# Kernel optimization log

Measured on AMD Instinct MI355X. Metric: run time of the kernel, lower is better.

The kernel has to match this reference:

```python
import jax, jax.numpy as jnp
import numpy as np

B, T, C, H = 4, 2048, 1024, 16
NEG = -1e9  # masked-fill value (finite to keep grads clean)


def setup_inputs() -> dict:
    key = jax.random.key(0)
    ks = jax.random.split(key, 5)
    s = 1.0 / np.sqrt(C)  # keep logits O(1) like trained linear layers
    return {
        "x": jax.random.normal(ks[0], (B, T, C), dtype=jnp.float32),
        "wq": jax.random.normal(ks[1], (C, C), dtype=jnp.float32) * s,
        "bq": jnp.zeros((C,), dtype=jnp.float32),
        "wk": jax.random.normal(ks[2], (C, C), dtype=jnp.float32) * s,
        "bk": jnp.zeros((C,), dtype=jnp.float32),
        "wv": jax.random.normal(ks[3], (C, C), dtype=jnp.float32) * s,
        "bv": jnp.zeros((C,), dtype=jnp.float32),
        "wo": jax.random.normal(ks[4], (C, C), dtype=jnp.float32) * s,
        "bo": jnp.zeros((C,), dtype=jnp.float32),
    }


def _split_heads(y):
    # [B,T,C] -> [B,H,T,hd]
    b, t, c = y.shape
    return y.reshape(b, t, H, c // H).transpose(0, 2, 1, 3)


def reference(x, wq, bq, wk, bk, wv, bv, wo, bo):
    b, t, c = x.shape
    scale = (c // H) ** (-0.5)
    q = _split_heads(x @ wq.T + bq)  # [B,H,T,hd]
    k = _split_heads(x @ wk.T + bk)
    v = _split_heads(x @ wv.T + bv)
    att = jnp.einsum("bhqd,bhkd->bhqk", q, k) * scale  # [B,H,T,T]
    causal = jnp.tril(jnp.ones((t, t), dtype=bool))
    att = jnp.where(causal[None, None], att, NEG)
    att = jax.nn.softmax(att, axis=-1)  # dropout is identity in eval mode
    y = jnp.einsum("bhqk,bhkd->bhqd", att, v)
    y = y.transpose(0, 2, 1, 3).reshape(b, t, c)
    return y @ wo.T + bo
```

## Files before the change

### kernel.cpp

```cpp
#include <hip/hip_runtime.h>


#define B_ 4
#define T_ 2048
#define C_ 1024
#define H_ 16
#define M_ 8192

typedef unsigned short u16;
typedef __bf16 bf16x8 __attribute__((ext_vector_type(8)));
typedef float f32x4 __attribute__((ext_vector_type(4)));

static __device__ __forceinline__ u16 f2bf(float f) {
  unsigned int u = __float_as_uint(f);
  u += 0x7fffu + ((u >> 16) & 1u);
  return (u16)(u >> 16);
}

static __device__ __forceinline__ void async16(const void* g, void* l) {
  __builtin_amdgcn_global_load_lds(
      (const __attribute__((address_space(1))) unsigned int*)g,
      (__attribute__((address_space(3))) unsigned int*)l, 16, 0, 0);
}

#if __has_builtin(__builtin_amdgcn_exp2f)
#define EXP2F(x) __builtin_amdgcn_exp2f(x)
#else
#define EXP2F(x) exp2f(x)
#endif

static __device__ __forceinline__ f32x4 mfma32(bf16x8 a, bf16x8 b, f32x4 c) {
  return __builtin_amdgcn_mfma_f32_16x16x32_bf16(a, b, c, 0, 0, 0);
}

__global__ __launch_bounds__(256) void cvt_x(const float* __restrict__ src,
                                             u16* __restrict__ dst, int n4) {
  int i = blockIdx.x * 256 + threadIdx.x;
  if (i >= n4) return;
  float4 f = ((const float4*)src)[i];
  ushort4 o;
  o.x = f2bf(f.x); o.y = f2bf(f.y); o.z = f2bf(f.z); o.w = f2bf(f.w);
  ((ushort4*)dst)[i] = o;
}

__global__ __launch_bounds__(256) void cvt_w4(const float* __restrict__ w0,
                                              const float* __restrict__ w1,
                                              const float* __restrict__ w2,
                                              const float* __restrict__ w3,
                                              u16* __restrict__ o0, u16* __restrict__ o1,
                                              u16* __restrict__ o2, u16* __restrict__ o3,
                                              float s0) {
  int i = blockIdx.x * 256 + threadIdx.x;
  const float* src; u16* dst; float s = 1.f;
  switch (blockIdx.y) {
    case 0: src = w0; dst = o0; s = s0; break;
    case 1: src = w1; dst = o1; break;
    case 2: src = w2; dst = o2; break;
    default: src = w3; dst = o3; break;
  }
  float4 f = ((const float4*)src)[i];
  ushort4 o;
  o.x = f2bf(f.x * s); o.y = f2bf(f.y * s); o.z = f2bf(f.z * s); o.w = f2bf(f.w * s);
  ((ushort4*)dst)[i] = o;
}

__global__ __launch_bounds__(256, 4) void gemm_qkv(const u16* __restrict__ A,
                                                   const u16* __restrict__ W,
                                                   const float* __restrict__ bq,
                                                   const float* __restrict__ bk,
                                                   const float* __restrict__ bv,
                                                   float qscale,
                                                   u16* __restrict__ outqk,
                                                   u16* __restrict__ vtb) {
  __shared__ __align__(16) union {
    struct { u16 A[128 * 64]; u16 B[128 * 64]; } s;
    u16 C[128 * 136];
  } sm;
  const int tid = threadIdx.x, lane = tid & 63, wave = tid >> 6;
  const int quad = lane >> 4, l16 = lane & 15;
  const int wm = wave >> 1, wn = wave & 1;
  const int sel = blockIdx.x >> 3;
  const int col0 = (blockIdx.x & 7) * 128, row0 = blockIdx.y * 128;
  const u16* Bt = W + (size_t)sel * C_ * C_;
  const float* bias = sel == 0 ? bq : (sel == 1 ? bk : bv);
  const float bscale = sel == 0 ? qscale : 1.f;

  f32x4 zero = {0.f, 0.f, 0.f, 0.f};
  f32x4 acc[4][4];
#pragma unroll
  for (int i = 0; i < 4; i++)
#pragma unroll
    for (int j = 0; j < 4; j++) acc[i][j] = zero;

  for (int k0 = 0; k0 < C_; k0 += 64) {
#pragma unroll
    for (int i = 0; i < 4; i++) {
      int c = i * 256 + tid;
      int r = c >> 3, gcc = (c & 7) ^ (r & 7);
      async16(A + (size_t)(row0 + r) * C_ + k0 + gcc * 8,
              sm.s.A + (size_t)(i * 256 + wave * 64) * 8);
      async16(Bt + (size_t)(col0 + r) * C_ + k0 + gcc * 8,
              sm.s.B + (size_t)(i * 256 + wave * 64) * 8);
    }
    __syncthreads();

#pragma unroll
    for (int kk = 0; kk < 2; kk++) {
      bf16x8 a[4], b[4];
#pragma unroll
      for (int i = 0; i < 4; i++) {
        int rm = wm * 64 + 16 * i + l16;
        a[i] = *(const bf16x8*)(sm.s.A + rm * 64 + (((kk * 4 + quad) ^ (rm & 7)) * 8));
        int rn = wn * 64 + 16 * i + l16;
        b[i] = *(const bf16x8*)(sm.s.B + rn * 64 + (((kk * 4 + quad) ^ (rn & 7)) * 8));
      }
#pragma unroll
      for (int i = 0; i < 4; i++)
#pragma unroll
        for (int j = 0; j < 4; j++)
          acc[i][j] = mfma32(a[i], b[j], acc[i][j]);
    }
    __syncthreads();
  }

  float bj[4];
#pragma unroll
  for (int j = 0; j < 4; j++) bj[j] = bias[col0 + wn * 64 + 16 * j + l16] * bscale;

  if (sel == 2) {
#pragma unroll
    for (int i = 0; i < 4; i++)
#pragma unroll
      for (int j = 0; j < 4; j++) {
        int cl = wn * 64 + 16 * j + l16;
        int rt = wm * 64 + 16 * i + quad * 4;
        union { u16 s[4]; uint2 u; } w;
#pragma unroll
        for (int r = 0; r < 4; r++) w.s[r] = f2bf(acc[i][j][r] + bj[j]);
        *(uint2*)(sm.C + (size_t)cl * 136 + rt) = w.u;
      }
    __syncthreads();
    const int bb = row0 >> 11, t0 = row0 & 2047;
#pragma unroll
    for (int c2 = 0; c2 < 8; c2++) {
      int c = c2 * 256 + tid;
      int nr = c >> 4, ch = c & 15;
      bf16x8 v = *(const bf16x8*)(sm.C + (size_t)nr * 136 + ch * 8);
      int gn = col0 + nr, d = gn & 63, hh = gn >> 6;
      *(bf16x8*)(vtb + ((size_t)((bb * 16 + hh) * 64 + d)) * T_ + t0 + ch * 8) = v;
    }
  } else {
#pragma unroll
    for (int i = 0; i < 4; i++)
#pragma unroll
      for (int j = 0; j < 4; j++) {
        int cl = wn * 64 + 16 * j + l16;
        int rt = wm * 64 + 16 * i + quad * 4;
#pragma unroll
        for (int r = 0; r < 4; r++)
          sm.C[(size_t)(rt + r) * 136 + cl] = f2bf(acc[i][j][r] + bj[j]);
      }
    __syncthreads();
    u16* dst = outqk + (size_t)sel * M_ * C_;
#pragma unroll
    for (int c2 = 0; c2 < 8; c2++) {
      int c = c2 * 256 + tid;
      int rw = c >> 4, ch = c & 15;
      bf16x8 v = *(const bf16x8*)(sm.C + (size_t)rw * 136 + ch * 8);
      *(bf16x8*)(dst + (size_t)(row0 + rw) * C_ + col0 + ch * 8) = v;
    }
  }
}

__global__ __launch_bounds__(256) void gemm_o(const u16* __restrict__ A,
                                              const u16* __restrict__ Bt,
                                              const float* __restrict__ bias,
                                              float* __restrict__ outf) {
  __shared__ __align__(16) u16 Asm[128 * 64];
  __shared__ __align__(16) u16 Bsm[128 * 64];
  const int tid = threadIdx.x, lane = tid & 63, wave = tid >> 6;
  const int quad = lane >> 4, l16 = lane & 15;
  const int wm = wave >> 1, wn = wave & 1;
  const int col0 = blockIdx.x * 128, row0 = blockIdx.y * 128;

  f32x4 zero = {0.f, 0.f, 0.f, 0.f};
  f32x4 acc[4][4];
#pragma unroll
  for (int i = 0; i < 4; i++)
#pragma unroll
    for (int j = 0; j < 4; j++) acc[i][j] = zero;

  for (int k0 = 0; k0 < C_; k0 += 64) {
#pragma unroll
    for (int i = 0; i < 4; i++) {
      int c = i * 256 + tid;
      int r = c >> 3, gcc = (c & 7) ^ (r & 7);
      async16(A + (size_t)(row0 + r) * C_ + k0 + gcc * 8,
              Asm + (size_t)(i * 256 + wave * 64) * 8);
      async16(Bt + (size_t)(col0 + r) * C_ + k0 + gcc * 8,
              Bsm + (size_t)(i * 256 + wave * 64) * 8);
    }
    __syncthreads();

#pragma unroll
    for (int kk = 0; kk < 2; kk++) {
      bf16x8 a[4], b[4];
#pragma unroll
      for (int i = 0; i < 4; i++) {
        int rm = wm * 64 + 16 * i + l16;
        a[i] = *(const bf16x8*)(Asm + rm * 64 + (((kk * 4 + quad) ^ (rm & 7)) * 8));
        int rn = wn * 64 + 16 * i + l16;
        b[i] = *(const bf16x8*)(Bsm + rn * 64 + (((kk * 4 + quad) ^ (rn & 7)) * 8));
      }
#pragma unroll
      for (int i = 0; i < 4; i++)
#pragma unroll
        for (int j = 0; j < 4; j++)
          acc[i][j] = mfma32(a[i], b[j], acc[i][j]);
    }
    __syncthreads();
  }

  float bj[4];
#pragma unroll
  for (int j = 0; j < 4; j++) bj[j] = bias[col0 + wn * 64 + 16 * j + l16];
#pragma unroll
  for (int i = 0; i < 4; i++) {
#pragma unroll
    for (int j = 0; j < 4; j++) {
      int gcol = col0 + wn * 64 + 16 * j + l16;
      int grow0 = row0 + wm * 64 + 16 * i + quad * 4;
#pragma unroll
      for (int r = 0; r < 4; r++)
        outf[(size_t)(grow0 + r) * C_ + gcol] = acc[i][j][r] + bj[j];
    }
  }
}

__global__ __launch_bounds__(256) void attn(const u16* __restrict__ q,
                                            const u16* __restrict__ k,
                                            const u16* __restrict__ vt,
                                            u16* __restrict__ y) {
  __shared__ __align__(16) u16 Ksm[64 * 64];
  __shared__ __align__(16) u16 Vsm[64 * 64];
  __shared__ __align__(16) u16 Psm[4][32 * 64];
  const int tid = threadIdx.x, lane = tid & 63, wave = tid >> 6;
  const int quad = lane >> 4, l16 = lane & 15;
  static const int qperm[16] = {15, 14, 11, 10, 12, 13, 8, 9, 3, 2, 7, 6, 0, 1, 4, 5};
  const int bh = blockIdx.x;
  const int qt = qperm[blockIdx.y];
  const int b = bh >> 4, h = bh & 15;
  const int jtN = 2 * qt + 2;
  const int jt_d = 2 * qt + (wave >> 1);

  bf16x8 qf[2][2];
#pragma unroll
  for (int m = 0; m < 2; m++) {
    const u16* qp =
        q + (size_t)(b * T_ + qt * 128 + wave * 32 + m * 16 + l16) * C_ + h * 64;
#pragma unroll
    for (int ks = 0; ks < 2; ks++)
      qf[m][ks] = *(const bf16x8*)(qp + ks * 32 + quad * 8);
  }

  f32x4 zero = {0.f, 0.f, 0.f, 0.f};
  f32x4 o[2][4];
  float lp[2][4];
#pragma unroll
  for (int m = 0; m < 2; m++) {
#pragma unroll
    for (int dt = 0; dt < 4; dt++) o[m][dt] = zero;
#pragma unroll
    for (int r = 0; r < 4; r++) lp[m][r] = 0.f;
  }

  const u16* kp[2];
  const u16* vp[2];
#pragma unroll
  for (int i = 0; i < 2; i++) {
    int c = i * 256 + tid;
    int r = c >> 3, lc = (c & 7) ^ (r & 7);
    kp[i] = k + (size_t)(b * T_ + r) * C_ + h * 64 + lc * 8;
    vp[i] = vt + (size_t)(bh * 64 + r) * T_ + lc * 8;
  }

  int qrel[2];
#pragma unroll
  for (int m = 0; m < 2; m++)
    qrel[m] = wave * 32 + m * 16 + quad * 4 - (wave >> 1) * 64 - l16;
  const int nlim0 = 2 * (wave & 1) + 1;

  u16* Pw = &Psm[wave][0];

#pragma unroll 1
  for (int jt = 0; jt < jtN; ++jt) {
#pragma unroll
    for (int i = 0; i < 2; i++) {
      async16(kp[i], Ksm + (size_t)(i * 256 + wave * 64) * 8);
      async16(vp[i], Vsm + (size_t)(i * 256 + wave * 64) * 8);
      kp[i] += (size_t)64 * C_;
      vp[i] += 64;
    }
    __syncthreads();

    if (jt <= jt_d) {
      const bool diag = (jt == jt_d);
#pragma unroll
      for (int n = 0; n < 4; ++n) {
        int rk = n * 16 + l16;
        bf16x8 kf0 = *(const bf16x8*)(Ksm + rk * 64 + ((quad ^ (rk & 7)) * 8));
        bf16x8 kf1 = *(const bf16x8*)(Ksm + rk * 64 + (((4 + quad) ^ (rk & 7)) * 8));
#pragma unroll
        for (int m = 0; m < 2; ++m) {
          if (!diag || n < nlim0 + m) {
            f32x4 s = mfma32(qf[m][0], kf0, zero);
            s = mfma32(qf[m][1], kf1, s);
            float e[4];
#pragma unroll
            for (int r = 0; r < 4; r++) e[r] = EXP2F(s[r]);
            if (diag) {
              int rmin = n * 16 - qrel[m];
#pragma unroll
              for (int r = 0; r < 4; r++)
                if (r < rmin) e[r] = 0.f;
            }
#pragma unroll
            for (int r = 0; r < 4; r++) {
              lp[m][r] += e[r];
              int qr = m * 16 + quad * 4 + r;
              Pw[qr * 64 + (((n * 2 + (l16 >> 3)) ^ (qr & 7)) * 8) + (l16 & 7)] =
                  f2bf(e[r]);
            }
          } else {
#pragma unroll
            for (int r = 0; r < 4; r++) {
              int qr = m * 16 + quad * 4 + r;
              Pw[qr * 64 + (((n * 2 + (l16 >> 3)) ^ (qr & 7)) * 8) + (l16 & 7)] = 0;
            }
          }
        }
      }
      bf16x8 pf[2][2];
#pragma unroll
      for (int m = 0; m < 2; m++)
#pragma unroll
        for (int ks = 0; ks < 2; ks++)
          pf[m][ks] = *(const bf16x8*)(Pw + (m * 16 + l16) * 64 +
                                       (((ks * 4 + quad) ^ (l16 & 7)) * 8));
#pragma unroll
      for (int dt = 0; dt < 4; ++dt) {
        int rv = dt * 16 + l16;
        bf16x8 vf0 = *(const bf16x8*)(Vsm + rv * 64 + ((quad ^ (rv & 7)) * 8));
        bf16x8 vf1 = *(const bf16x8*)(Vsm + rv * 64 + (((4 + quad) ^ (rv & 7)) * 8));
#pragma unroll
        for (int m = 0; m < 2; m++) {
          o[m][dt] = mfma32(pf[m][0], vf0, o[m][dt]);
          o[m][dt] = mfma32(pf[m][1], vf1, o[m][dt]);
        }
      }
    }
    __syncthreads();
  }

#pragma unroll
  for (int m = 0; m < 2; m++)
#pragma unroll
    for (int r = 0; r < 4; r++) {
      float v = lp[m][r];
      v += __shfl_xor(v, 1);
      v += __shfl_xor(v, 2);
      v += __shfl_xor(v, 4);
      v += __shfl_xor(v, 8);
      lp[m][r] = 1.f / v;
    }

#pragma unroll
  for (int m = 0; m < 2; m++)
#pragma unroll
    for (int r = 0; r < 4; r++) {
      int grow = b * T_ + qt * 128 + wave * 32 + m * 16 + quad * 4 + r;
#pragma unroll
      for (int dt = 0; dt < 4; dt++)
        y[(size_t)grow * C_ + h * 64 + dt * 16 + l16] = f2bf(o[m][dt][r] * lp[m][r]);
    }
}

extern "C" void kernel_launch(void* const* d_in, const int* in_sizes, int n_in,
                              void* d_out, int out_size, void* d_ws, size_t ws_size,
                              hipStream_t stream) {
  const float* x  = (const float*)d_in[0];
  const float* wq = (const float*)d_in[1];
  const float* bq = (const float*)d_in[2];
  const float* wk = (const float*)d_in[3];
  const float* bk = (const float*)d_in[4];
  const float* wv = (const float*)d_in[5];
  const float* bv = (const float*)d_in[6];
  const float* wo = (const float*)d_in[7];
  const float* bo = (const float*)d_in[8];
  float* out = (float*)d_out;

  const float QSCALE = 0.125f * 1.4426950408889634f;

  u16* xb  = (u16*)d_ws;
  u16* wqb = xb  + (size_t)M_ * C_;
  u16* wkb = wqb + (size_t)C_ * C_;
  u16* wvb = wkb + (size_t)C_ * C_;
  u16* wob = wvb + (size_t)C_ * C_;
  u16* qb  = wob + (size_t)C_ * C_;
  u16* kb  = qb  + (size_t)M_ * C_;
  u16* vtb = kb  + (size_t)M_ * C_;
  u16* yb  = xb;

  cvt_x<<<M_ * C_ / 4 / 256, 256, 0, stream>>>(x, xb, M_ * C_ / 4);
  cvt_w4<<<dim3(C_ * C_ / 4 / 256, 4), 256, 0, stream>>>(
      wq, wk, wv, wo, wqb, wkb, wvb, wob, QSCALE);

  gemm_qkv<<<dim3(24, M_ / 128), 256, 0, stream>>>(xb, wqb, bq, bk, bv, QSCALE,
                                                   qb, vtb);

  attn<<<dim3(B_ * H_, 16), 256, 0, stream>>>(qb, kb, vtb, yb);

  gemm_o<<<dim3(C_ / 128, M_ / 128), 256, 0, stream>>>(yb, wob, bo, out);
}
```

Baseline: 269.9 us.

## Widen attention KV tile to 128 keys and fuse conversion kernels into one

The attention kernel now loads 128 keys per iteration, split into two 64-key halves, instead of 64. This halves the number of loop iterations and the barrier pairs per query tile, and the causal diagonal logic is rebuilt around per-wave half-tile limits. Separately, the x and weight bf16 conversions are merged into a single launch to save one kernel launch. The larger shared K/V buffers raise LDS use per block, which may lower occupancy.

```diff
diff --git a/kernel.cpp b/kernel.cpp
--- a/kernel.cpp
+++ b/kernel.cpp
@@ -33,35 +33,34 @@
   return __builtin_amdgcn_mfma_f32_16x16x32_bf16(a, b, c, 0, 0, 0);
 }
 
-__global__ __launch_bounds__(256) void cvt_x(const float* __restrict__ src,
-                                             u16* __restrict__ dst, int n4) {
+__global__ __launch_bounds__(256) void cvt_all(const float* __restrict__ x,
+                                               const float* __restrict__ w0,
+                                               const float* __restrict__ w1,
+                                               const float* __restrict__ w2,
+                                               const float* __restrict__ w3,
+                                               u16* __restrict__ xb,
+                                               u16* __restrict__ wb,
+                                               float s0) {
+  const int NX = M_ * C_ / 4, NW = C_ * C_ / 4;
   int i = blockIdx.x * 256 + threadIdx.x;
-  if (i >= n4) return;
-  float4 f = ((const float4*)src)[i];
-  ushort4 o;
-  o.x = f2bf(f.x); o.y = f2bf(f.y); o.z = f2bf(f.z); o.w = f2bf(f.w);
-  ((ushort4*)dst)[i] = o;
-}
-
-__global__ __launch_bounds__(256) void cvt_w4(const float* __restrict__ w0,
-                                              const float* __restrict__ w1,
-                                              const float* __restrict__ w2,
-                                              const float* __restrict__ w3,
-                                              u16* __restrict__ o0, u16* __restrict__ o1,
-                                              u16* __restrict__ o2, u16* __restrict__ o3,
-                                              float s0) {
-  int i = blockIdx.x * 256 + threadIdx.x;
-  const float* src; u16* dst; float s = 1.f;
-  switch (blockIdx.y) {
-    case 0: src = w0; dst = o0; s = s0; break;
-    case 1: src = w1; dst = o1; break;
-    case 2: src = w2; dst = o2; break;
-    default: src = w3; dst = o3; break;
-  }
-  float4 f = ((const float4*)src)[i];
+  const float* src;
+  u16* dst;
+  int idx;
+  float s = 1.f;
+  if (i < NX) {
+    src = x; dst = xb; idx = i;
+  } else {
+    int j = i - NX;
+    int w = j / NW;
+    idx = j - w * NW;
+    src = (w == 0) ? w0 : (w == 1) ? w1 : (w == 2) ? w2 : w3;
+    dst = wb + (size_t)w * C_ * C_;
+    if (w == 0) s = s0;
+  }
+  float4 f = ((const float4*)src)[idx];
   ushort4 o;
   o.x = f2bf(f.x * s); o.y = f2bf(f.y * s); o.z = f2bf(f.z * s); o.w = f2bf(f.w * s);
-  ((ushort4*)dst)[i] = o;
+  ((ushort4*)dst)[idx] = o;
 }
 
 __global__ __launch_bounds__(256, 4) void gemm_qkv(const u16* __restrict__ A,
@@ -241,8 +240,8 @@
                                             const u16* __restrict__ k,
                                             const u16* __restrict__ vt,
                                             u16* __restrict__ y) {
-  __shared__ __align__(16) u16 Ksm[64 * 64];
-  __shared__ __align__(16) u16 Vsm[64 * 64];
+  __shared__ __align__(16) u16 Ksm[128 * 64];
+  __shared__ __align__(16) u16 Vsm[2][64 * 64];
   __shared__ __align__(16) u16 Psm[4][32 * 64];
   const int tid = threadIdx.x, lane = tid & 63, wave = tid >> 6;
   const int quad = lane >> 4, l16 = lane & 15;
@@ -250,8 +249,6 @@
   const int bh = blockIdx.x;
   const int qt = qperm[blockIdx.y];
   const int b = bh >> 4, h = bh & 15;
-  const int jtN = 2 * qt + 2;
-  const int jt_d = 2 * qt + (wave >> 1);
 
   bf16x8 qf[2][2];
 #pragma unroll
@@ -274,52 +271,66 @@
     for (int r = 0; r < 4; r++) lp[m][r] = 0.f;
   }
 
-  const u16* kp[2];
-  const u16* vp[2];
-#pragma unroll
-  for (int i = 0; i < 2; i++) {
+  const u16* kp[4];
+  const u16* vp[4];
+#pragma unroll
+  for (int i = 0; i < 4; i++) {
     int c = i * 256 + tid;
     int r = c >> 3, lc = (c & 7) ^ (r & 7);
     kp[i] = k + (size_t)(b * T_ + r) * C_ + h * 64 + lc * 8;
-    vp[i] = vt + (size_t)(bh * 64 + r) * T_ + lc * 8;
-  }
+  }
+#pragma unroll
+  for (int s = 0; s < 2; s++)
+#pragma unroll
+    for (int i = 0; i < 2; i++) {
+      int c = i * 256 + tid;
+      int r = c >> 3, lc = (c & 7) ^ (r & 7);
+      vp[s * 2 + i] = vt + (size_t)(bh * 64 + r) * T_ + 64 * s + lc * 8;
+    }
 
   int qrel[2];
 #pragma unroll
   for (int m = 0; m < 2; m++)
-    qrel[m] = wave * 32 + m * 16 + quad * 4 - (wave >> 1) * 64 - l16;
-  const int nlim0 = 2 * (wave & 1) + 1;
+    qrel[m] = wave * 32 + m * 16 + quad * 4 - l16;
 
   u16* Pw = &Psm[wave][0];
 
 #pragma unroll 1
-  for (int jt = 0; jt < jtN; ++jt) {
-#pragma unroll
-    for (int i = 0; i < 2; i++) {
+  for (int jt = 0; jt <= qt; ++jt) {
+#pragma unroll
+    for (int i = 0; i < 4; i++) {
       async16(kp[i], Ksm + (size_t)(i * 256 + wave * 64) * 8);
-      async16(vp[i], Vsm + (size_t)(i * 256 + wave * 64) * 8);
-      kp[i] += (size_t)64 * C_;
-      vp[i] += 64;
-    }
-    __syncthreads();
-
-    if (jt <= jt_d) {
-      const bool diag = (jt == jt_d);
+      kp[i] += (size_t)128 * C_;
+    }
+#pragma unroll
+    for (int s = 0; s < 2; s++)
+#pragma unroll
+      for (int i = 0; i < 2; i++) {
+        async16(vp[s * 2 + i], Vsm[s] + (size_t)(i * 256 + wave * 64) * 8);
+        vp[s * 2 + i] += 128;
+      }
+    __syncthreads();
+
+    const bool diag = (jt == qt);
+#pragma unroll
+    for (int hh = 0; hh < 2; ++hh) {
+      if (diag && (2 * wave + 2 - 4 * hh) <= 0) continue;
 #pragma unroll
       for (int n = 0; n < 4; ++n) {
-        int rk = n * 16 + l16;
+        int rk = hh * 64 + n * 16 + l16;
         bf16x8 kf0 = *(const bf16x8*)(Ksm + rk * 64 + ((quad ^ (rk & 7)) * 8));
         bf16x8 kf1 = *(const bf16x8*)(Ksm + rk * 64 + (((4 + quad) ^ (rk & 7)) * 8));
 #pragma unroll
         for (int m = 0; m < 2; ++m) {
-          if (!diag || n < nlim0 + m) {
+          int nlim = diag ? (2 * wave + m + 1 - 4 * hh) : 4;
+          if (n < nlim) {
             f32x4 s = mfma32(qf[m][0], kf0, zero);
             s = mfma32(qf[m][1], kf1, s);
             float e[4];
 #pragma unroll
             for (int r = 0; r < 4; r++) e[r] = EXP2F(s[r]);
             if (diag) {
-              int rmin = n * 16 - qrel[m];
+              int rmin = hh * 64 + n * 16 - qrel[m];
 #pragma unroll
               for (int r = 0; r < 4; r++)
                 if (r < rmin) e[r] = 0.f;
@@ -350,8 +361,8 @@
 #pragma unroll
       for (int dt = 0; dt < 4; ++dt) {
         int rv = dt * 16 + l16;
-        bf16x8 vf0 = *(const bf16x8*)(Vsm + rv * 64 + ((quad ^ (rv & 7)) * 8));
-        bf16x8 vf1 = *(const bf16x8*)(Vsm + rv * 64 + (((4 + quad) ^ (rv & 7)) * 8));
+        bf16x8 vf0 = *(const bf16x8*)(Vsm[hh] + rv * 64 + ((quad ^ (rv & 7)) * 8));
+        bf16x8 vf1 = *(const bf16x8*)(Vsm[hh] + rv * 64 + (((4 + quad) ^ (rv & 7)) * 8));
 #pragma unroll
         for (int m = 0; m < 2; m++) {
           o[m][dt] = mfma32(pf[m][0], vf0, o[m][dt]);
@@ -403,17 +414,14 @@
 
   u16* xb  = (u16*)d_ws;
   u16* wqb = xb  + (size_t)M_ * C_;
-  u16* wkb = wqb + (size_t)C_ * C_;
-  u16* wvb = wkb + (size_t)C_ * C_;
-  u16* wob = wvb + (size_t)C_ * C_;
+  u16* wob = wqb + 3 * (size_t)C_ * C_;
   u16* qb  = wob + (size_t)C_ * C_;
   u16* kb  = qb  + (size_t)M_ * C_;
   u16* vtb = kb  + (size_t)M_ * C_;
   u16* yb  = xb;
 
-  cvt_x<<<M_ * C_ / 4 / 256, 256, 0, stream>>>(x, xb, M_ * C_ / 4);
-  cvt_w4<<<dim3(C_ * C_ / 4 / 256, 4), 256, 0, stream>>>(
-      wq, wk, wv, wo, wqb, wkb, wvb, wob, QSCALE);
+  const int NCVT = (M_ * C_ + 4 * C_ * C_) / 4 / 256;
+  cvt_all<<<NCVT, 256, 0, stream>>>(x, wq, wk, wv, wo, xb, wqb, QSCALE);
 
   gemm_qkv<<<dim3(24, M_ / 128), 256, 0, stream>>>(xb, wqb, bq, bk, bv, QSCALE,
                                                    qb, vtb);
```

New measurement: 272.8 us. Within noise of the previous version (+1.1%).
